# Kernel optimization log

Measured on AMD Instinct MI355X. Metric: run time of the kernel, lower is better.

Reference implementation:

```python
import jax, jax.numpy as jnp
import numpy as np

N_NODES = 50000
N_EDGES = 600000
D_IN = 128
D_HID = 128


def _gcn_layer(x, src, dst, W, b, n):
    # PyG GCNConv: h = x @ W; add self-loops; symmetric normalization
    # out_i = sum_j (d_i^-1/2 d_j^-1/2) h_j + (d_i^-1) h_i + b, with d = deg + 1
    h = x @ W  # [N, F]
    ones = jnp.ones(src.shape[0], dtype=x.dtype)
    deg = jax.ops.segment_sum(ones, dst, num_segments=n) + jnp.asarray(1.0, x.dtype)
    dinv = jax.lax.rsqrt(deg)  # [N]
    coef = dinv[src] * dinv[dst]  # [E]
    msg = h[src] * coef[:, None]  # gather + scale, [E, F]
    agg = jax.ops.segment_sum(msg, dst, num_segments=n)  # scatter-add, [N, F]
    agg = agg + h * (dinv * dinv)[:, None]  # self-loop contribution
    return agg + b


def setup_inputs() -> dict:
    key = jax.random.key(0)
    k1, k2, k3, k4 = jax.random.split(key, 4)
    x = jax.random.normal(k1, (N_NODES, D_IN), dtype=jnp.float32)
    edge_index = jax.random.randint(k2, (2, N_EDGES), 0, N_NODES, dtype=jnp.int32)
    # Glorot-ish init for linear weights
    W1 = jax.random.normal(k3, (D_IN, D_HID), dtype=jnp.float32) / np.sqrt(D_IN)
    W2 = jax.random.normal(k4, (D_HID, D_HID), dtype=jnp.float32) / np.sqrt(D_HID)
    b1 = jnp.zeros((D_HID,), dtype=jnp.float32)
    b2 = jnp.zeros((D_HID,), dtype=jnp.float32)
    return {"x": x, "edge_index": edge_index, "W1": W1, "b1": b1, "W2": W2, "b2": b2}


def reference(x, edge_index, W1, b1, W2, b2):
    src = edge_index[0]
    dst = edge_index[1]
    n = x.shape[0]
    h = _gcn_layer(x, src, dst, W1, b1, n)
    h = jax.nn.relu(h)
    out = _gcn_layer(h, src, dst, W2, b2, n)
    return out
```

## Files before the change

kernel.cpp:

```cpp
#include <hip/hip_runtime.h>
#include <hip/hip_bf16.h>

typedef __attribute__((ext_vector_type(8))) short short8;
typedef __attribute__((ext_vector_type(4))) float floatx4;

#define D 128
#define BCAP 2048
#define CPAD 16
#define NBIN 256
#define EPBMAX 2560

__device__ __forceinline__ unsigned short f2bf(float f) {
    unsigned u = __float_as_uint(f);
    u += 0x7FFFu + ((u >> 16) & 1u);
    return (unsigned short)(u >> 16);
}
__device__ __forceinline__ float bf2f(unsigned short h) {
    return __uint_as_float(((unsigned)h) << 16);
}
__device__ __forceinline__ float bflo(unsigned p) { return __uint_as_float(p << 16); }
__device__ __forceinline__ float bfhi(unsigned p) { return __uint_as_float(p & 0xFFFF0000u); }

__device__ __forceinline__ int block_excl_scan256(int v, int* lds, int tid) {
    int lane = tid & 63, wid = tid >> 6;
    int x = v;
    #pragma unroll
    for (int d = 1; d < 64; d <<= 1) {
        int y = __shfl_up(x, d, 64);
        if (lane >= d) x += y;
    }
    if (lane == 63) lds[wid] = x;
    __syncthreads();
    if (tid == 0) {
        int run = 0;
        #pragma unroll
        for (int i = 0; i < 4; i++) { int t2 = lds[i]; lds[i] = run; run += t2; }
    }
    __syncthreads();
    return lds[wid] + x - v;
}

__global__ __launch_bounds__(256) void bucket_wconv_kernel(const int* __restrict__ src,
                                                           const int* __restrict__ dst,
                                                           int* __restrict__ bcnt,
                                                           unsigned* __restrict__ bucket, int E,
                                                           const float* __restrict__ W1,
                                                           const float* __restrict__ W2,
                                                           unsigned short* __restrict__ whi1,
                                                           unsigned short* __restrict__ wlo1,
                                                           unsigned short* __restrict__ whi2,
                                                           unsigned short* __restrict__ wlo2,
                                                           int nbuk) {
    int b = blockIdx.x;
    if (b >= NBIN) {
        int gid = (b - NBIN) * 256 + threadIdx.x;
        int which = gid >> 14;
        int tid = gid & 16383;
        const float* W = which ? W2 : W1;
        unsigned short* whi = which ? whi2 : whi1;
        unsigned short* wlo = which ? wlo2 : wlo1;
        int j    = tid & 7;
        int col  = (tid >> 3) & 127;
        int quad = (tid >> 10) & 3;
        int kb   = tid >> 12;
        float wv = W[(kb * 32 + quad * 8 + j) * D + col];
        unsigned u = __float_as_uint(wv);
        unsigned short h = (unsigned short)(u >> 16);
        whi[tid] = h;
        wlo[tid] = f2bf(wv - bf2f(h));
        return;
    }
    __shared__ unsigned lent[EPBMAX];
    __shared__ unsigned sorted_e[EPBMAX];
    __shared__ int sdst[EPBMAX];
    __shared__ unsigned short loff[EPBMAX];
    __shared__ unsigned char lbkt[EPBMAX];
    __shared__ int hist[256];
    __shared__ int lstart[256];
    __shared__ int gbase[256];
    __shared__ int lds4[4];

    int tid = threadIdx.x;
    int sub = b & 7;
    int epb = (E + NBIN - 1) / NBIN;
    int beg = b * epb;
    int cnt = E - beg;
    if (cnt > epb) cnt = epb;
    if (cnt < 0) cnt = 0;

    hist[tid] = 0;
    __syncthreads();

    for (int i = tid; i < cnt; i += 256) {
        int dd = dst[beg + i], ss = src[beg + i];
        int bk = dd >> 8;
        lent[i] = ((unsigned)(dd & 255) << 16) | (unsigned)ss;
        lbkt[i] = (unsigned char)bk;
        loff[i] = (unsigned short)atomicAdd(&hist[bk], 1);
    }
    __syncthreads();

    int h = hist[tid];
    int ex = block_excl_scan256(h, lds4, tid);
    lstart[tid] = ex;
    if (tid < nbuk && h > 0)
        gbase[tid] = atomicAdd(&bcnt[(tid * 8 + sub) * CPAD], h);
    __syncthreads();

    for (int i = tid; i < cnt; i += 256) {
        int bk = lbkt[i];
        int of = loff[i];
        int lp = lstart[bk] + of;
        int gp = gbase[bk] + of;
        sorted_e[lp] = lent[i];
        sdst[lp] = (gp < BCAP) ? ((bk * 8 + sub) * BCAP + gp) : -1;
    }
    __syncthreads();

    for (int i = tid; i < cnt; i += 256) {
        int dsti = sdst[i];
        if (dsti >= 0) bucket[dsti] = sorted_e[i];
    }
}

__global__ __launch_bounds__(256) void build_gemm_kernel(const unsigned* __restrict__ bucket,
                                                         const int* __restrict__ bcnt,
                                                         int* __restrict__ row_ptr,
                                                         float* __restrict__ dinv,
                                                         int* __restrict__ esrc, int N, int E,
                                                         const float* __restrict__ A,
                                                         const unsigned short* __restrict__ whi,
                                                         const unsigned short* __restrict__ wlo,
                                                         unsigned short* __restrict__ C, int M,
                                                         int nbuk) {
    __shared__ int lds4[4];
    __shared__ int sbase[256];
    __shared__ int hist[256];
    __shared__ int cur[256];
    int tid = threadIdx.x;
    int b = blockIdx.x;
    if (b < nbuk) {
        int tot = 0;
        if (tid < nbuk) {
            #pragma unroll
            for (int s = 0; s < 8; s++) tot += min(bcnt[(tid * 8 + s) * CPAD], BCAP);
        }
        int ex = block_excl_scan256(tot, lds4, tid);
        sbase[tid] = ex;
        hist[tid] = 0;
        __syncthreads();
        int base = sbase[b];
        for (int sub = 0; sub < 8; sub++) {
            int cnt = min(bcnt[(b * 8 + sub) * CPAD], BCAP);
            const unsigned* bp = bucket + (size_t)(b * 8 + sub) * BCAP;
            for (int i = tid; i < cnt; i += 256)
                atomicAdd(&hist[bp[i] >> 16], 1);
        }
        __syncthreads();
        int h = hist[tid];
        int off = block_excl_scan256(h, lds4, tid);
        cur[tid] = base + off;
        int node = b * 256 + tid;
        if (node < N) {
            row_ptr[node] = base + off;
            dinv[node] = rsqrtf((float)(h + 1));
        }
        if (b == 0 && tid == 0) row_ptr[N] = E;
        __syncthreads();
        for (int sub = 0; sub < 8; sub++) {
            int cnt = min(bcnt[(b * 8 + sub) * CPAD], BCAP);
            const unsigned* bp = bucket + (size_t)(b * 8 + sub) * BCAP;
            for (int i = tid; i < cnt; i += 256) {
                unsigned v = bp[i];
                int p = atomicAdd(&cur[v >> 16], 1);
                esrc[p] = (int)(v & 0xFFFFu);
            }
        }
        return;
    }
    int lane = tid & 63, wid = tid >> 6;
    int quad = lane >> 4, l15 = lane & 15;
    int row0 = (b - nbuk) * 64;
    int n0 = wid * 32;

    short8 bhi[2][4], blo[2][4];
    #pragma unroll
    for (int t = 0; t < 2; t++)
        #pragma unroll
        for (int kb = 0; kb < 4; kb++) {
            size_t base = ((size_t)((kb * 4 + quad) * 128 + (n0 + t * 16 + l15))) * 8;
            bhi[t][kb] = *reinterpret_cast<const short8*>(whi + base);
            blo[t][kb] = *reinterpret_cast<const short8*>(wlo + base);
        }

    #pragma unroll
    for (int rg = 0; rg < 4; rg++) {
        int r0 = row0 + rg * 16;
        int ar = r0 + l15; if (ar > M - 1) ar = M - 1;
        short8 ahi[4], alo[4];
        #pragma unroll
        for (int kb = 0; kb < 4; kb++) {
            const float4* ap = reinterpret_cast<const float4*>(A + (size_t)ar * D + kb * 32 + quad * 8);
            float4 v0 = ap[0], v1 = ap[1];
            float vv[8] = {v0.x, v0.y, v0.z, v0.w, v1.x, v1.y, v1.z, v1.w};
            short8 vh, vl;
            #pragma unroll
            for (int j = 0; j < 8; j++) {
                unsigned u = __float_as_uint(vv[j]);
                unsigned short h = (unsigned short)(u >> 16);
                vh[j] = (short)h;
                vl[j] = (short)f2bf(vv[j] - bf2f(h));
            }
            ahi[kb] = vh;
            alo[kb] = vl;
        }
        floatx4 acc0 = {0.f, 0.f, 0.f, 0.f};
        floatx4 acc1 = {0.f, 0.f, 0.f, 0.f};
        #pragma unroll
        for (int kb = 0; kb < 4; kb++) {
            acc0 = __builtin_amdgcn_mfma_f32_16x16x32_bf16(ahi[kb], bhi[0][kb], acc0, 0, 0, 0);
            acc1 = __builtin_amdgcn_mfma_f32_16x16x32_bf16(ahi[kb], bhi[1][kb], acc1, 0, 0, 0);
            acc0 = __builtin_amdgcn_mfma_f32_16x16x32_bf16(ahi[kb], blo[0][kb], acc0, 0, 0, 0);
            acc1 = __builtin_amdgcn_mfma_f32_16x16x32_bf16(ahi[kb], blo[1][kb], acc1, 0, 0, 0);
            acc0 = __builtin_amdgcn_mfma_f32_16x16x32_bf16(alo[kb], bhi[0][kb], acc0, 0, 0, 0);
            acc1 = __builtin_amdgcn_mfma_f32_16x16x32_bf16(alo[kb], bhi[1][kb], acc1, 0, 0, 0);
        }
        #pragma unroll
        for (int r = 0; r < 4; r++) {
            int orow = r0 + quad * 4 + r;
            if (orow < M) {
                C[(size_t)orow * D + n0 + l15]      = f2bf(acc0[r]);
                C[(size_t)orow * D + n0 + 16 + l15] = f2bf(acc1[r]);
            }
        }
    }
}

__device__ __forceinline__ void agg_qbody(const uint4* __restrict__ H4,
                                          const float* __restrict__ dinv,
                                          const int* __restrict__ row_ptr,
                                          const int* __restrict__ esrc,
                                          const float* __restrict__ bias,
                                          int node, int fl, float* acc) {
    #pragma unroll
    for (int j = 0; j < 8; j++) acc[j] = 0.f;
    int beg = row_ptr[node], end = row_ptr[node + 1];
    int e = beg;
    for (; e + 4 <= end; e += 4) {
        int s0 = esrc[e], s1 = esrc[e + 1], s2 = esrc[e + 2], s3 = esrc[e + 3];
        float c0 = dinv[s0], c1 = dinv[s1], c2 = dinv[s2], c3 = dinv[s3];
        uint4 p0 = H4[(size_t)s0 * 16 + fl];
        uint4 p1 = H4[(size_t)s1 * 16 + fl];
        uint4 p2 = H4[(size_t)s2 * 16 + fl];
        uint4 p3 = H4[(size_t)s3 * 16 + fl];
        acc[0] += c0 * bflo(p0.x) + c1 * bflo(p1.x) + c2 * bflo(p2.x) + c3 * bflo(p3.x);
        acc[1] += c0 * bfhi(p0.x) + c1 * bfhi(p1.x) + c2 * bfhi(p2.x) + c3 * bfhi(p3.x);
        acc[2] += c0 * bflo(p0.y) + c1 * bflo(p1.y) + c2 * bflo(p2.y) + c3 * bflo(p3.y);
        acc[3] += c0 * bfhi(p0.y) + c1 * bfhi(p1.y) + c2 * bfhi(p2.y) + c3 * bfhi(p3.y);
        acc[4] += c0 * bflo(p0.z) + c1 * bflo(p1.z) + c2 * bflo(p2.z) + c3 * bflo(p3.z);
        acc[5] += c0 * bfhi(p0.z) + c1 * bfhi(p1.z) + c2 * bfhi(p2.z) + c3 * bfhi(p3.z);
        acc[6] += c0 * bflo(p0.w) + c1 * bflo(p1.w) + c2 * bflo(p2.w) + c3 * bflo(p3.w);
        acc[7] += c0 * bfhi(p0.w) + c1 * bfhi(p1.w) + c2 * bfhi(p2.w) + c3 * bfhi(p3.w);
    }
    for (; e < end; e++) {
        int s0 = esrc[e];
        float c = dinv[s0];
        uint4 p0 = H4[(size_t)s0 * 16 + fl];
        acc[0] += c * bflo(p0.x); acc[1] += c * bfhi(p0.x);
        acc[2] += c * bflo(p0.y); acc[3] += c * bfhi(p0.y);
        acc[4] += c * bflo(p0.z); acc[5] += c * bfhi(p0.z);
        acc[6] += c * bflo(p0.w); acc[7] += c * bfhi(p0.w);
    }
    float di = dinv[node];
    float dii = di * di;
    uint4 ps = H4[(size_t)node * 16 + fl];
    const float4* b4 = (const float4*)bias;
    float4 bb0 = b4[fl * 2], bb1 = b4[fl * 2 + 1];
    #pragma unroll
    for (int j = 0; j < 8; j++) acc[j] *= di;
    acc[0] += dii * bflo(ps.x) + bb0.x;
    acc[1] += dii * bfhi(ps.x) + bb0.y;
    acc[2] += dii * bflo(ps.y) + bb0.z;
    acc[3] += dii * bfhi(ps.y) + bb0.w;
    acc[4] += dii * bflo(ps.z) + bb1.x;
    acc[5] += dii * bfhi(ps.z) + bb1.y;
    acc[6] += dii * bflo(ps.w) + bb1.z;
    acc[7] += dii * bfhi(ps.w) + bb1.w;
}

__global__ __launch_bounds__(256) void agg_gemm2_kernel(const unsigned short* __restrict__ H,
                                                        const float* __restrict__ dinv,
                                                        const int* __restrict__ row_ptr,
                                                        const int* __restrict__ esrc,
                                                        const float* __restrict__ bias,
                                                        const unsigned short* __restrict__ whi,
                                                        const unsigned short* __restrict__ wlo,
                                                        unsigned short* __restrict__ C, int N) {
    __shared__ unsigned short Asm[16 * 136];
    int tid = threadIdx.x;
    int node0 = blockIdx.x * 16;
    int r = tid >> 4;
    int fl = tid & 15;
    int node = node0 + r;
    float acc[8];
    if (node < N) {
        agg_qbody((const uint4*)H, dinv, row_ptr, esrc, bias, node, fl, acc);
    } else {
        #pragma unroll
        for (int j = 0; j < 8; j++) acc[j] = 0.f;
    }
    short8 a;
    #pragma unroll
    for (int j = 0; j < 8; j++) a[j] = (short)f2bf(fmaxf(acc[j], 0.f));
    *reinterpret_cast<short8*>(&Asm[r * 136 + fl * 8]) = a;
    __syncthreads();

    int lane = tid & 63, wid = tid >> 6;
    int quad = lane >> 4, l15 = lane & 15;
    int n0 = wid * 32;
    floatx4 acc0 = {0.f, 0.f, 0.f, 0.f};
    floatx4 acc1 = {0.f, 0.f, 0.f, 0.f};
    #pragma unroll 1
    for (int kb = 0; kb < 4; kb++) {
        size_t wb = ((size_t)((kb * 4 + quad) * 128 + (n0 + l15))) * 8;
        short8 bh0 = *reinterpret_cast<const short8*>(whi + wb);
        short8 bh1 = *reinterpret_cast<const short8*>(whi + wb + 128);
        short8 bl0 = *reinterpret_cast<const short8*>(wlo + wb);
        short8 bl1 = *reinterpret_cast<const short8*>(wlo + wb + 128);
        short8 af = *reinterpret_cast<const short8*>(&Asm[l15 * 136 + kb * 32 + quad * 8]);
        acc0 = __builtin_amdgcn_mfma_f32_16x16x32_bf16(af, bh0, acc0, 0, 0, 0);
        acc1 = __builtin_amdgcn_mfma_f32_16x16x32_bf16(af, bh1, acc1, 0, 0, 0);
        acc0 = __builtin_amdgcn_mfma_f32_16x16x32_bf16(af, bl0, acc0, 0, 0, 0);
        acc1 = __builtin_amdgcn_mfma_f32_16x16x32_bf16(af, bl1, acc1, 0, 0, 0);
    }
    #pragma unroll
    for (int rr = 0; rr < 4; rr++) {
        int orow = node0 + quad * 4 + rr;
        if (orow < N) {
            float dv = dinv[orow];
            C[(size_t)orow * D + n0 + l15]      = f2bf(dv * acc0[rr]);
            C[(size_t)orow * D + n0 + 16 + l15] = f2bf(dv * acc1[rr]);
        }
    }
}

__global__ __launch_bounds__(256) void agg_sum_f32out_kernel(const unsigned short* __restrict__ H,
                                                             const float* __restrict__ dinv,
                                                             const int* __restrict__ row_ptr,
                                                             const int* __restrict__ esrc,
                                                             const float* __restrict__ bias,
                                                             float4* __restrict__ out, int N) {
    int node = blockIdx.x * 16 + (threadIdx.x >> 4);
    int fl = threadIdx.x & 15;
    if (node >= N) return;
    const uint4* H4 = (const uint4*)H;
    float acc[8];
    #pragma unroll
    for (int j = 0; j < 8; j++) acc[j] = 0.f;
    int beg = row_ptr[node], end = row_ptr[node + 1];
    int e = beg;
    for (; e + 4 <= end; e += 4) {
        int s0 = esrc[e], s1 = esrc[e + 1], s2 = esrc[e + 2], s3 = esrc[e + 3];
        uint4 p0 = H4[(size_t)s0 * 16 + fl];
        uint4 p1 = H4[(size_t)s1 * 16 + fl];
        uint4 p2 = H4[(size_t)s2 * 16 + fl];
        uint4 p3 = H4[(size_t)s3 * 16 + fl];
        acc[0] += bflo(p0.x) + bflo(p1.x) + bflo(p2.x) + bflo(p3.x);
        acc[1] += bfhi(p0.x) + bfhi(p1.x) + bfhi(p2.x) + bfhi(p3.x);
        acc[2] += bflo(p0.y) + bflo(p1.y) + bflo(p2.y) + bflo(p3.y);
        acc[3] += bfhi(p0.y) + bfhi(p1.y) + bfhi(p2.y) + bfhi(p3.y);
        acc[4] += bflo(p0.z) + bflo(p1.z) + bflo(p2.z) + bflo(p3.z);
        acc[5] += bfhi(p0.z) + bfhi(p1.z) + bfhi(p2.z) + bfhi(p3.z);
        acc[6] += bflo(p0.w) + bflo(p1.w) + bflo(p2.w) + bflo(p3.w);
        acc[7] += bfhi(p0.w) + bfhi(p1.w) + bfhi(p2.w) + bfhi(p3.w);
    }
    for (; e < end; e++) {
        int s0 = esrc[e];
        uint4 p0 = H4[(size_t)s0 * 16 + fl];
        acc[0] += bflo(p0.x); acc[1] += bfhi(p0.x);
        acc[2] += bflo(p0.y); acc[3] += bfhi(p0.y);
        acc[4] += bflo(p0.z); acc[5] += bfhi(p0.z);
        acc[6] += bflo(p0.w); acc[7] += bfhi(p0.w);
    }
    uint4 ps = H4[(size_t)node * 16 + fl];
    acc[0] += bflo(ps.x); acc[1] += bfhi(ps.x);
    acc[2] += bflo(ps.y); acc[3] += bfhi(ps.y);
    acc[4] += bflo(ps.z); acc[5] += bfhi(ps.z);
    acc[6] += bflo(ps.w); acc[7] += bfhi(ps.w);
    float di = dinv[node];
    const float4* b4 = (const float4*)bias;
    float4 bb0 = b4[fl * 2], bb1 = b4[fl * 2 + 1];
    float4 o0, o1;
    o0.x = di * acc[0] + bb0.x; o0.y = di * acc[1] + bb0.y;
    o0.z = di * acc[2] + bb0.z; o0.w = di * acc[3] + bb0.w;
    o1.x = di * acc[4] + bb1.x; o1.y = di * acc[5] + bb1.y;
    o1.z = di * acc[6] + bb1.z; o1.w = di * acc[7] + bb1.w;
    out[(size_t)node * 32 + fl * 2]     = o0;
    out[(size_t)node * 32 + fl * 2 + 1] = o1;
}

extern "C" void kernel_launch(void* const* d_in, const int* in_sizes, int n_in,
                              void* d_out, int out_size, void* d_ws, size_t ws_size,
                              hipStream_t stream) {
    const float* x  = (const float*)d_in[0];
    const int*   ei = (const int*)d_in[1];
    const float* W1 = (const float*)d_in[2];
    const float* b1 = (const float*)d_in[3];
    const float* W2 = (const float*)d_in[4];
    const float* b2 = (const float*)d_in[5];

    int N = in_sizes[0] / D;
    int E = in_sizes[1] / 2;
    const int* src = ei;
    const int* dst = ei + E;

    int nbuk = (N + 255) / 256;

    char* ws = (char*)d_ws;
    int*      bcnt   = (int*)(ws + 0);
    unsigned* bucket = (unsigned*)(ws + 102400);
    int*      row_ptr= (int*)(ws + 12947456);
    float*    dinv   = (float*)(ws + 13147520);
    int*      esrcs  = (int*)(ws + 13347520);
    unsigned short* whi1 = (unsigned short*)(ws + 15747584);
    unsigned short* wlo1 = (unsigned short*)(ws + 15780352);
    unsigned short* whi2 = (unsigned short*)(ws + 15813120);
    unsigned short* wlo2 = (unsigned short*)(ws + 15845888);
    unsigned short* hfeat = (unsigned short*)(ws + 15878656);
    unsigned short* h2    = (unsigned short*)(ws + 28678656);

    int gb   = (N + 63) / 64;
    int ab16 = (N + 15) / 16;

    hipMemsetAsync(bcnt, 0, 102400, stream);
    bucket_wconv_kernel<<<NBIN + 128, 256, 0, stream>>>(src, dst, bcnt, bucket, E,
                                                        W1, W2, whi1, wlo1, whi2, wlo2, nbuk);

    build_gemm_kernel<<<nbuk + gb, 256, 0, stream>>>(bucket, bcnt, row_ptr, dinv, esrcs,
                                                     N, E, x, whi1, wlo1, hfeat, N, nbuk);

    agg_gemm2_kernel<<<ab16, 256, 0, stream>>>(hfeat, dinv, row_ptr, esrcs, b1,
                                               whi2, wlo2, h2, N);

    agg_sum_f32out_kernel<<<ab16, 256, 0, stream>>>(h2, dinv, row_ptr, esrcs, b2,
                                                    (float4*)d_out, N);
}
```

Measured before the change: 168.8 us.

## Split each node's edge list across two thread halves in aggregation kernels

Both aggregation kernels now give each node 32 threads instead of 16. The two halves take alternating groups of 4 edges and combine their partial sums with a cross-lane shuffle. The GEMM stage of the fused kernel now runs on 8 waves, each computing a 16-column slice. The goal is more memory-level parallelism and shorter per-thread serial gather chains on the irregular neighbor loads, at the cost of more threads, shuffle overhead and duplicated epilogue work.

```diff
diff --git a/kernel.cpp b/kernel.cpp
--- a/kernel.cpp
+++ b/kernel.cpp
@@ -236,130 +236,54 @@
     }
 }
 
-__device__ __forceinline__ void agg_qbody(const uint4* __restrict__ H4,
-                                          const float* __restrict__ dinv,
-                                          const int* __restrict__ row_ptr,
-                                          const int* __restrict__ esrc,
-                                          const float* __restrict__ bias,
-                                          int node, int fl, float* acc) {
+#define ACC4(c0, p0, c1, p1, c2, p2, c3, p3) \
+    acc[0] += c0 * bflo(p0.x) + c1 * bflo(p1.x) + c2 * bflo(p2.x) + c3 * bflo(p3.x); \
+    acc[1] += c0 * bfhi(p0.x) + c1 * bfhi(p1.x) + c2 * bfhi(p2.x) + c3 * bfhi(p3.x); \
+    acc[2] += c0 * bflo(p0.y) + c1 * bflo(p1.y) + c2 * bflo(p2.y) + c3 * bflo(p3.y); \
+    acc[3] += c0 * bfhi(p0.y) + c1 * bfhi(p1.y) + c2 * bfhi(p2.y) + c3 * bfhi(p3.y); \
+    acc[4] += c0 * bflo(p0.z) + c1 * bflo(p1.z) + c2 * bflo(p2.z) + c3 * bflo(p3.z); \
+    acc[5] += c0 * bfhi(p0.z) + c1 * bfhi(p1.z) + c2 * bfhi(p2.z) + c3 * bfhi(p3.z); \
+    acc[6] += c0 * bflo(p0.w) + c1 * bflo(p1.w) + c2 * bflo(p2.w) + c3 * bflo(p3.w); \
+    acc[7] += c0 * bfhi(p0.w) + c1 * bfhi(p1.w) + c2 * bfhi(p2.w) + c3 * bfhi(p3.w);
+
+
+__device__ __forceinline__ void agg_half_w(const uint4* __restrict__ H4,
+                                           const float* __restrict__ dinv,
+                                           const int* __restrict__ esrc,
+                                           int beg, int end, int half, int fl, float* acc) {
     #pragma unroll
     for (int j = 0; j < 8; j++) acc[j] = 0.f;
-    int beg = row_ptr[node], end = row_ptr[node + 1];
-    int e = beg;
-    for (; e + 4 <= end; e += 4) {
+    int e = beg + half * 4;
+    for (; e + 4 <= end; e += 8) {
         int s0 = esrc[e], s1 = esrc[e + 1], s2 = esrc[e + 2], s3 = esrc[e + 3];
         float c0 = dinv[s0], c1 = dinv[s1], c2 = dinv[s2], c3 = dinv[s3];
         uint4 p0 = H4[(size_t)s0 * 16 + fl];
         uint4 p1 = H4[(size_t)s1 * 16 + fl];
         uint4 p2 = H4[(size_t)s2 * 16 + fl];
         uint4 p3 = H4[(size_t)s3 * 16 + fl];
-        acc[0] += c0 * bflo(p0.x) + c1 * bflo(p1.x) + c2 * bflo(p2.x) + c3 * bflo(p3.x);
-        acc[1] += c0 * bfhi(p0.x) + c1 * bfhi(p1.x) + c2 * bfhi(p2.x) + c3 * bfhi(p3.x);
-        acc[2] += c0 * bflo(p0.y) + c1 * bflo(p1.y) + c2 * bflo(p2.y) + c3 * bflo(p3.y);
-        acc[3] += c0 * bfhi(p0.y) + c1 * bfhi(p1.y) + c2 * bfhi(p2.y) + c3 * bfhi(p3.y);
-        acc[4] += c0 * bflo(p0.z) + c1 * bflo(p1.z) + c2 * bflo(p2.z) + c3 * bflo(p3.z);
-        acc[5] += c0 * bfhi(p0.z) + c1 * bfhi(p1.z) + c2 * bfhi(p2.z) + c3 * bfhi(p3.z);
-        acc[6] += c0 * bflo(p0.w) + c1 * bflo(p1.w) + c2 * bflo(p2.w) + c3 * bflo(p3.w);
-        acc[7] += c0 * bfhi(p0.w) + c1 * bfhi(p1.w) + c2 * bfhi(p2.w) + c3 * bfhi(p3.w);
-    }
-    for (; e < end; e++) {
-        int s0 = esrc[e];
-        float c = dinv[s0];
-        uint4 p0 = H4[(size_t)s0 * 16 + fl];
-        acc[0] += c * bflo(p0.x); acc[1] += c * bfhi(p0.x);
-        acc[2] += c * bflo(p0.y); acc[3] += c * bfhi(p0.y);
-        acc[4] += c * bflo(p0.z); acc[5] += c * bfhi(p0.z);
-        acc[6] += c * bflo(p0.w); acc[7] += c * bfhi(p0.w);
-    }
-    float di = dinv[node];
-    float dii = di * di;
-    uint4 ps = H4[(size_t)node * 16 + fl];
-    const float4* b4 = (const float4*)bias;
-    float4 bb0 = b4[fl * 2], bb1 = b4[fl * 2 + 1];
-    #pragma unroll
-    for (int j = 0; j < 8; j++) acc[j] *= di;
-    acc[0] += dii * bflo(ps.x) + bb0.x;
-    acc[1] += dii * bfhi(ps.x) + bb0.y;
-    acc[2] += dii * bflo(ps.y) + bb0.z;
-    acc[3] += dii * bfhi(ps.y) + bb0.w;
-    acc[4] += dii * bflo(ps.z) + bb1.x;
-    acc[5] += dii * bfhi(ps.z) + bb1.y;
-    acc[6] += dii * bflo(ps.w) + bb1.z;
-    acc[7] += dii * bfhi(ps.w) + bb1.w;
-}
-
-__global__ __launch_bounds__(256) void agg_gemm2_kernel(const unsigned short* __restrict__ H,
-                                                        const float* __restrict__ dinv,
-                                                        const int* __restrict__ row_ptr,
-                                                        const int* __restrict__ esrc,
-                                                        const float* __restrict__ bias,
-                                                        const unsigned short* __restrict__ whi,
-                                                        const unsigned short* __restrict__ wlo,
-                                                        unsigned short* __restrict__ C, int N) {
-    __shared__ unsigned short Asm[16 * 136];
-    int tid = threadIdx.x;
-    int node0 = blockIdx.x * 16;
-    int r = tid >> 4;
-    int fl = tid & 15;
-    int node = node0 + r;
-    float acc[8];
-    if (node < N) {
-        agg_qbody((const uint4*)H, dinv, row_ptr, esrc, bias, node, fl, acc);
-    } else {
-        #pragma unroll
-        for (int j = 0; j < 8; j++) acc[j] = 0.f;
-    }
-    short8 a;
-    #pragma unroll
-    for (int j = 0; j < 8; j++) a[j] = (short)f2bf(fmaxf(acc[j], 0.f));
-    *reinterpret_cast<short8*>(&Asm[r * 136 + fl * 8]) = a;
-    __syncthreads();
-
-    int lane = tid & 63, wid = tid >> 6;
-    int quad = lane >> 4, l15 = lane & 15;
-    int n0 = wid * 32;
-    floatx4 acc0 = {0.f, 0.f, 0.f, 0.f};
-    floatx4 acc1 = {0.f, 0.f, 0.f, 0.f};
-    #pragma unroll 1
-    for (int kb = 0; kb < 4; kb++) {
-        size_t wb = ((size_t)((kb * 4 + quad) * 128 + (n0 + l15))) * 8;
-        short8 bh0 = *reinterpret_cast<const short8*>(whi + wb);
-        short8 bh1 = *reinterpret_cast<const short8*>(whi + wb + 128);
-        short8 bl0 = *reinterpret_cast<const short8*>(wlo + wb);
-        short8 bl1 = *reinterpret_cast<const short8*>(wlo + wb + 128);
-        short8 af = *reinterpret_cast<const short8*>(&Asm[l15 * 136 + kb * 32 + quad * 8]);
-        acc0 = __builtin_amdgcn_mfma_f32_16x16x32_bf16(af, bh0, acc0, 0, 0, 0);
-        acc1 = __builtin_amdgcn_mfma_f32_16x16x32_bf16(af, bh1, acc1, 0, 0, 0);
-        acc0 = __builtin_amdgcn_mfma_f32_16x16x32_bf16(af, bl0, acc0, 0, 0, 0);
-        acc1 = __builtin_amdgcn_mfma_f32_16x16x32_bf16(af, bl1, acc1, 0, 0, 0);
-    }
-    #pragma unroll
-    for (int rr = 0; rr < 4; rr++) {
-        int orow = node0 + quad * 4 + rr;
-        if (orow < N) {
-            float dv = dinv[orow];
-            C[(size_t)orow * D + n0 + l15]      = f2bf(dv * acc0[rr]);
-            C[(size_t)orow * D + n0 + 16 + l15] = f2bf(dv * acc1[rr]);
-        }
-    }
-}
-
-__global__ __launch_bounds__(256) void agg_sum_f32out_kernel(const unsigned short* __restrict__ H,
-                                                             const float* __restrict__ dinv,
-                                                             const int* __restrict__ row_ptr,
-                                                             const int* __restrict__ esrc,
-                                                             const float* __restrict__ bias,
-                                                             float4* __restrict__ out, int N) {
-    int node = blockIdx.x * 16 + (threadIdx.x >> 4);
-    int fl = threadIdx.x & 15;
-    if (node >= N) return;
-    const uint4* H4 = (const uint4*)H;
-    float acc[8];
+        ACC4(c0, p0, c1, p1, c2, p2, c3, p3);
+    }
+    int Q = (end - beg) >> 2;
+    if (half == (Q & 1)) {
+        for (int t = beg + 4 * Q; t < end; t++) {
+            int s0 = esrc[t];
+            float c = dinv[s0];
+            uint4 p0 = H4[(size_t)s0 * 16 + fl];
+            acc[0] += c * bflo(p0.x); acc[1] += c * bfhi(p0.x);
+            acc[2] += c * bflo(p0.y); acc[3] += c * bfhi(p0.y);
+            acc[4] += c * bflo(p0.z); acc[5] += c * bfhi(p0.z);
+            acc[6] += c * bflo(p0.w); acc[7] += c * bfhi(p0.w);
+        }
+    }
+}
+
+__device__ __forceinline__ void agg_half_s(const uint4* __restrict__ H4,
+                                           const int* __restrict__ esrc,
+                                           int beg, int end, int half, int fl, float* acc) {
     #pragma unroll
     for (int j = 0; j < 8; j++) acc[j] = 0.f;
-    int beg = row_ptr[node], end = row_ptr[node + 1];
-    int e = beg;
-    for (; e + 4 <= end; e += 4) {
+    int e = beg + half * 4;
+    for (; e + 4 <= end; e += 8) {
         int s0 = esrc[e], s1 = esrc[e + 1], s2 = esrc[e + 2], s3 = esrc[e + 3];
         uint4 p0 = H4[(size_t)s0 * 16 + fl];
         uint4 p1 = H4[(size_t)s1 * 16 + fl];
@@ -374,14 +298,112 @@
         acc[6] += bflo(p0.w) + bflo(p1.w) + bflo(p2.w) + bflo(p3.w);
         acc[7] += bfhi(p0.w) + bfhi(p1.w) + bfhi(p2.w) + bfhi(p3.w);
     }
-    for (; e < end; e++) {
-        int s0 = esrc[e];
-        uint4 p0 = H4[(size_t)s0 * 16 + fl];
-        acc[0] += bflo(p0.x); acc[1] += bfhi(p0.x);
-        acc[2] += bflo(p0.y); acc[3] += bfhi(p0.y);
-        acc[4] += bflo(p0.z); acc[5] += bfhi(p0.z);
-        acc[6] += bflo(p0.w); acc[7] += bfhi(p0.w);
-    }
+    int Q = (end - beg) >> 2;
+    if (half == (Q & 1)) {
+        for (int t = beg + 4 * Q; t < end; t++) {
+            int s0 = esrc[t];
+            uint4 p0 = H4[(size_t)s0 * 16 + fl];
+            acc[0] += bflo(p0.x); acc[1] += bfhi(p0.x);
+            acc[2] += bflo(p0.y); acc[3] += bfhi(p0.y);
+            acc[4] += bflo(p0.z); acc[5] += bfhi(p0.z);
+            acc[6] += bflo(p0.w); acc[7] += bfhi(p0.w);
+        }
+    }
+}
+
+__global__ __launch_bounds__(512) void agg_gemm2_kernel(const unsigned short* __restrict__ H,
+                                                        const float* __restrict__ dinv,
+                                                        const int* __restrict__ row_ptr,
+                                                        const int* __restrict__ esrc,
+                                                        const float* __restrict__ bias,
+                                                        const unsigned short* __restrict__ whi,
+                                                        const unsigned short* __restrict__ wlo,
+                                                        unsigned short* __restrict__ C, int N) {
+    __shared__ unsigned short Asm[16 * 136];
+    int tid = threadIdx.x;
+    int node0 = blockIdx.x * 16;
+    int r = tid >> 5;
+    int half = (tid >> 4) & 1;
+    int fl = tid & 15;
+    int node = node0 + r;
+    float acc[8];
+    #pragma unroll
+    for (int j = 0; j < 8; j++) acc[j] = 0.f;
+    if (node < N) {
+        int beg = row_ptr[node], end = row_ptr[node + 1];
+        agg_half_w((const uint4*)H, dinv, esrc, beg, end, half, fl, acc);
+    }
+    #pragma unroll
+    for (int j = 0; j < 8; j++) acc[j] += __shfl_xor(acc[j], 16);
+    if (node < N) {
+        float di = dinv[node];
+        float dii = di * di;
+        uint4 ps = ((const uint4*)H)[(size_t)node * 16 + fl];
+        const float4* b4 = (const float4*)bias;
+        float4 bb0 = b4[fl * 2], bb1 = b4[fl * 2 + 1];
+        #pragma unroll
+        for (int j = 0; j < 8; j++) acc[j] *= di;
+        acc[0] += dii * bflo(ps.x) + bb0.x;
+        acc[1] += dii * bfhi(ps.x) + bb0.y;
+        acc[2] += dii * bflo(ps.y) + bb0.z;
+        acc[3] += dii * bfhi(ps.y) + bb0.w;
+        acc[4] += dii * bflo(ps.z) + bb1.x;
+        acc[5] += dii * bfhi(ps.z) + bb1.y;
+        acc[6] += dii * bflo(ps.w) + bb1.z;
+        acc[7] += dii * bfhi(ps.w) + bb1.w;
+    }
+    if (half == 0) {
+        short8 a;
+        #pragma unroll
+        for (int j = 0; j < 8; j++) a[j] = (short)f2bf(fmaxf(acc[j], 0.f));
+        *reinterpret_cast<short8*>(&Asm[r * 136 + fl * 8]) = a;
+    }
+    __syncthreads();
+
+    int lane = tid & 63, wid = tid >> 6;
+    int quad = lane >> 4, l15 = lane & 15;
+    int n0 = wid * 16;
+    floatx4 acc0 = {0.f, 0.f, 0.f, 0.f};
+    #pragma unroll 1
+    for (int kb = 0; kb < 4; kb++) {
+        size_t wb = ((size_t)((kb * 4 + quad) * 128 + (n0 + l15))) * 8;
+        short8 bh = *reinterpret_cast<const short8*>(whi + wb);
+        short8 bl = *reinterpret_cast<const short8*>(wlo + wb);
+        short8 af = *reinterpret_cast<const short8*>(&Asm[l15 * 136 + kb * 32 + quad * 8]);
+        acc0 = __builtin_amdgcn_mfma_f32_16x16x32_bf16(af, bh, acc0, 0, 0, 0);
+        acc0 = __builtin_amdgcn_mfma_f32_16x16x32_bf16(af, bl, acc0, 0, 0, 0);
+    }
+    #pragma unroll
+    for (int rr = 0; rr < 4; rr++) {
+        int orow = node0 + quad * 4 + rr;
+        if (orow < N) {
+            float dv = dinv[orow];
+            C[(size_t)orow * D + n0 + l15] = f2bf(dv * acc0[rr]);
+        }
+    }
+}
+
+__global__ __launch_bounds__(256) void agg_sum_f32out_kernel(const unsigned short* __restrict__ H,
+                                                             const float* __restrict__ dinv,
+                                                             const int* __restrict__ row_ptr,
+                                                             const int* __restrict__ esrc,
+                                                             const float* __restrict__ bias,
+                                                             float4* __restrict__ out, int N) {
+    int tid = threadIdx.x;
+    int node = blockIdx.x * 8 + (tid >> 5);
+    int half = (tid >> 4) & 1;
+    int fl = tid & 15;
+    const uint4* H4 = (const uint4*)H;
+    float acc[8];
+    #pragma unroll
+    for (int j = 0; j < 8; j++) acc[j] = 0.f;
+    if (node < N) {
+        int beg = row_ptr[node], end = row_ptr[node + 1];
+        agg_half_s(H4, esrc, beg, end, half, fl, acc);
+    }
+    #pragma unroll
+    for (int j = 0; j < 8; j++) acc[j] += __shfl_xor(acc[j], 16);
+    if (node >= N) return;
     uint4 ps = H4[(size_t)node * 16 + fl];
     acc[0] += bflo(ps.x); acc[1] += bfhi(ps.x);
     acc[2] += bflo(ps.y); acc[3] += bfhi(ps.y);
@@ -389,14 +411,19 @@
     acc[6] += bflo(ps.w); acc[7] += bfhi(ps.w);
     float di = dinv[node];
     const float4* b4 = (const float4*)bias;
-    float4 bb0 = b4[fl * 2], bb1 = b4[fl * 2 + 1];
-    float4 o0, o1;
-    o0.x = di * acc[0] + bb0.x; o0.y = di * acc[1] + bb0.y;
-    o0.z = di * acc[2] + bb0.z; o0.w = di * acc[3] + bb0.w;
-    o1.x = di * acc[4] + bb1.x; o1.y = di * acc[5] + bb1.y;
-    o1.z = di * acc[6] + bb1.z; o1.w = di * acc[7] + bb1.w;
-    out[(size_t)node * 32 + fl * 2]     = o0;
-    out[(size_t)node * 32 + fl * 2 + 1] = o1;
+    if (half == 0) {
+        float4 bb0 = b4[fl * 2];
+        float4 o0;
+        o0.x = di * acc[0] + bb0.x; o0.y = di * acc[1] + bb0.y;
+        o0.z = di * acc[2] + bb0.z; o0.w = di * acc[3] + bb0.w;
+        out[(size_t)node * 32 + fl * 2] = o0;
+    } else {
+        float4 bb1 = b4[fl * 2 + 1];
+        float4 o1;
+        o1.x = di * acc[4] + bb1.x; o1.y = di * acc[5] + bb1.y;
+        o1.z = di * acc[6] + bb1.z; o1.w = di * acc[7] + bb1.w;
+        out[(size_t)node * 32 + fl * 2 + 1] = o1;
+    }
 }
 
 extern "C" void kernel_launch(void* const* d_in, const int* in_sizes, int n_in,
@@ -429,8 +456,9 @@
     unsigned short* hfeat = (unsigned short*)(ws + 15878656);
     unsigned short* h2    = (unsigned short*)(ws + 28678656);
 
-    int gb   = (N + 63) / 64;
-    int ab16 = (N + 15) / 16;
+    int gb    = (N + 63) / 64;
+    int ag16  = (N + 15) / 16;
+    int ag8   = (N + 7) / 8;
 
     hipMemsetAsync(bcnt, 0, 102400, stream);
     bucket_wconv_kernel<<<NBIN + 128, 256, 0, stream>>>(src, dst, bcnt, bucket, E,
@@ -439,9 +467,9 @@
     build_gemm_kernel<<<nbuk + gb, 256, 0, stream>>>(bucket, bcnt, row_ptr, dinv, esrcs,
                                                      N, E, x, whi1, wlo1, hfeat, N, nbuk);
 
-    agg_gemm2_kernel<<<ab16, 256, 0, stream>>>(hfeat, dinv, row_ptr, esrcs, b1,
+    agg_gemm2_kernel<<<ag16, 512, 0, stream>>>(hfeat, dinv, row_ptr, esrcs, b1,
                                                whi2, wlo2, h2, N);
 
-    agg_sum_f32out_kernel<<<ab16, 256, 0, stream>>>(h2, dinv, row_ptr, esrcs, b2,
-                                                    (float4*)d_out, N);
-}
+    agg_sum_f32out_kernel<<<ag8, 256, 0, stream>>>(h2, dinv, row_ptr, esrcs, b2,
+                                                   (float4*)d_out, N);
+}
```

Measured after the change: 179.2 us. 6.1% more time.

## Group nodes by in-degree class to balance aggregation work across blocks

Applied to the files above, without the earlier changes.

While building the CSR, the build kernel bins each node into one of 32 degree classes and writes a permutation array grouped by class. Both aggregation kernels then map each slot to a node through that permutation, so each block of 16 nodes holds rows of similar degree, which is meant to reduce divergence and load imbalance in the edge loops. BCAP is also halved, which shrinks the workspace but relies on each sub-bucket holding at most 1024 edges. The cost is an indirect node lookup, a per-block class prefix scan, scattered output rows, and worse locality from the permuted node order.

```diff
diff --git a/kernel.cpp b/kernel.cpp
--- a/kernel.cpp
+++ b/kernel.cpp
@@ -5,10 +5,11 @@
 typedef __attribute__((ext_vector_type(4))) float floatx4;
 
 #define D 128
-#define BCAP 2048
+#define BCAP 1024
 #define CPAD 16
 #define NBIN 256
 #define EPBMAX 2560
+#define NCLS 32
 
 __device__ __forceinline__ unsigned short f2bf(float f) {
     unsigned u = __float_as_uint(f);
@@ -132,11 +133,15 @@
                                                          const unsigned short* __restrict__ whi,
                                                          const unsigned short* __restrict__ wlo,
                                                          unsigned short* __restrict__ C, int M,
+                                                         int* __restrict__ ccnt,
+                                                         int* __restrict__ pclass,
                                                          int nbuk) {
     __shared__ int lds4[4];
     __shared__ int sbase[256];
     __shared__ int hist[256];
     __shared__ int cur[256];
+    __shared__ int chist[NCLS];
+    __shared__ int cbase_l[NCLS];
     int tid = threadIdx.x;
     int b = blockIdx.x;
     if (b < nbuk) {
@@ -148,6 +153,7 @@
         int ex = block_excl_scan256(tot, lds4, tid);
         sbase[tid] = ex;
         hist[tid] = 0;
+        if (tid < NCLS) chist[tid] = 0;
         __syncthreads();
         int base = sbase[b];
         for (int sub = 0; sub < 8; sub++) {
@@ -161,12 +167,19 @@
         int off = block_excl_scan256(h, lds4, tid);
         cur[tid] = base + off;
         int node = b * 256 + tid;
+        int cls = -1, cpos = 0;
         if (node < N) {
             row_ptr[node] = base + off;
             dinv[node] = rsqrtf((float)(h + 1));
+            cls = min(h, NCLS - 1);
+            cpos = atomicAdd(&chist[cls], 1);
         }
         if (b == 0 && tid == 0) row_ptr[N] = E;
         __syncthreads();
+        if (tid < NCLS && chist[tid] > 0)
+            cbase_l[tid] = atomicAdd(&ccnt[tid * CPAD], chist[tid]);
+        __syncthreads();
+        if (node < N) pclass[cls * N + cbase_l[cls] + cpos] = node;
         for (int sub = 0; sub < 8; sub++) {
             int cnt = min(bcnt[(b * 8 + sub) * CPAD], BCAP);
             const unsigned* bp = bucket + (size_t)(b * 8 + sub) * BCAP;
@@ -288,6 +301,28 @@
     acc[7] += dii * bfhi(ps.w) + bb1.w;
 }
 
+__device__ __forceinline__ void load_class_prefix(const int* __restrict__ ccnt,
+                                                  int* cpre, int tid) {
+    if (tid < NCLS) {
+        int v = ccnt[tid * CPAD];
+        #pragma unroll
+        for (int d = 1; d < NCLS; d <<= 1) {
+            int y = __shfl_up(v, d, 64);
+            if (tid >= d) v += y;
+        }
+        cpre[tid + 1] = v;
+        if (tid == 0) cpre[0] = 0;
+    }
+}
+
+__device__ __forceinline__ int slot_to_node(const int* cpre,
+                                            const int* __restrict__ pclass,
+                                            int g, int N) {
+    int c = 0;
+    while (c < NCLS - 1 && g >= cpre[c + 1]) c++;
+    return pclass[c * N + (g - cpre[c])];
+}
+
 __global__ __launch_bounds__(256) void agg_gemm2_kernel(const unsigned short* __restrict__ H,
                                                         const float* __restrict__ dinv,
                                                         const int* __restrict__ row_ptr,
@@ -295,15 +330,25 @@
                                                         const float* __restrict__ bias,
                                                         const unsigned short* __restrict__ whi,
                                                         const unsigned short* __restrict__ wlo,
-                                                        unsigned short* __restrict__ C, int N) {
+                                                        unsigned short* __restrict__ C,
+                                                        const int* __restrict__ ccnt,
+                                                        const int* __restrict__ pclass, int N) {
     __shared__ unsigned short Asm[16 * 136];
+    __shared__ int cpre[NCLS + 1];
+    __shared__ int nidL[16];
     int tid = threadIdx.x;
+    load_class_prefix(ccnt, cpre, tid);
+    __syncthreads();
     int node0 = blockIdx.x * 16;
     int r = tid >> 4;
     int fl = tid & 15;
-    int node = node0 + r;
+    int g = node0 + r;
+    int node = 0;
+    bool valid = (g < N);
+    if (valid) node = slot_to_node(cpre, pclass, g, N);
+    if (fl == 0) nidL[r] = valid ? node : -1;
     float acc[8];
-    if (node < N) {
+    if (valid) {
         agg_qbody((const uint4*)H, dinv, row_ptr, esrc, bias, node, fl, acc);
     } else {
         #pragma unroll
@@ -335,8 +380,9 @@
     }
     #pragma unroll
     for (int rr = 0; rr < 4; rr++) {
-        int orow = node0 + quad * 4 + rr;
-        if (orow < N) {
+        int os = quad * 4 + rr;
+        if (node0 + os < N) {
+            int orow = nidL[os];
             float dv = dinv[orow];
             C[(size_t)orow * D + n0 + l15]      = f2bf(dv * acc0[rr]);
             C[(size_t)orow * D + n0 + 16 + l15] = f2bf(dv * acc1[rr]);
@@ -349,10 +395,17 @@
                                                              const int* __restrict__ row_ptr,
                                                              const int* __restrict__ esrc,
                                                              const float* __restrict__ bias,
-                                                             float4* __restrict__ out, int N) {
-    int node = blockIdx.x * 16 + (threadIdx.x >> 4);
-    int fl = threadIdx.x & 15;
-    if (node >= N) return;
+                                                             float4* __restrict__ out,
+                                                             const int* __restrict__ ccnt,
+                                                             const int* __restrict__ pclass, int N) {
+    __shared__ int cpre[NCLS + 1];
+    int tid = threadIdx.x;
+    load_class_prefix(ccnt, cpre, tid);
+    __syncthreads();
+    int g = blockIdx.x * 16 + (tid >> 4);
+    int fl = tid & 15;
+    if (g >= N) return;
+    int node = slot_to_node(cpre, pclass, g, N);
     const uint4* H4 = (const uint4*)H;
     float acc[8];
     #pragma unroll
@@ -418,30 +471,33 @@
 
     char* ws = (char*)d_ws;
     int*      bcnt   = (int*)(ws + 0);
+    int*      ccnt   = (int*)(ws + 100352);
     unsigned* bucket = (unsigned*)(ws + 102400);
-    int*      row_ptr= (int*)(ws + 12947456);
-    float*    dinv   = (float*)(ws + 13147520);
-    int*      esrcs  = (int*)(ws + 13347520);
-    unsigned short* whi1 = (unsigned short*)(ws + 15747584);
-    unsigned short* wlo1 = (unsigned short*)(ws + 15780352);
-    unsigned short* whi2 = (unsigned short*)(ws + 15813120);
-    unsigned short* wlo2 = (unsigned short*)(ws + 15845888);
-    unsigned short* hfeat = (unsigned short*)(ws + 15878656);
-    unsigned short* h2    = (unsigned short*)(ws + 28678656);
+    int*      row_ptr= (int*)(ws + 6524928);
+    float*    dinv   = (float*)(ws + 6729728);
+    int*      esrcs  = (int*)(ws + 6929728);
+    unsigned short* whi1 = (unsigned short*)(ws + 9329728);
+    unsigned short* wlo1 = (unsigned short*)(ws + 9362496);
+    unsigned short* whi2 = (unsigned short*)(ws + 9395264);
+    unsigned short* wlo2 = (unsigned short*)(ws + 9428032);
+    unsigned short* hfeat = (unsigned short*)(ws + 9460800);
+    unsigned short* h2    = (unsigned short*)(ws + 22260800);
+    int*      pclass = (int*)(ws + 35060800);
 
     int gb   = (N + 63) / 64;
     int ab16 = (N + 15) / 16;
 
-    hipMemsetAsync(bcnt, 0, 102400, stream);
+    hipMemsetAsync(ws, 0, 102400, stream);
     bucket_wconv_kernel<<<NBIN + 128, 256, 0, stream>>>(src, dst, bcnt, bucket, E,
                                                         W1, W2, whi1, wlo1, whi2, wlo2, nbuk);
 
     build_gemm_kernel<<<nbuk + gb, 256, 0, stream>>>(bucket, bcnt, row_ptr, dinv, esrcs,
-                                                     N, E, x, whi1, wlo1, hfeat, N, nbuk);
+                                                     N, E, x, whi1, wlo1, hfeat, N,
+                                                     ccnt, pclass, nbuk);
 
     agg_gemm2_kernel<<<ab16, 256, 0, stream>>>(hfeat, dinv, row_ptr, esrcs, b1,
-                                               whi2, wlo2, h2, N);
+                                               whi2, wlo2, h2, ccnt, pclass, N);
 
     agg_sum_f32out_kernel<<<ab16, 256, 0, stream>>>(h2, dinv, row_ptr, esrcs, b2,
-                                                    (float4*)d_out, N);
-}
+                                                    (float4*)d_out, ccnt, pclass, N);
+}
```

New measurement: 188.6 us. +11.7%, slower.
